# Kernel tuning notes

Measured on AMD Instinct MI355X. Metric: run time of the kernel, lower is better.

## Reference

```python
import jax, jax.numpy as jnp
from jax import lax
import numpy as np

DN = ('NDHWC', 'DHWIO', 'NDHWC')

def _conv(x, W):
    # stride-1 kernel-3 sparse conv on dense grid: SAME conv; absent voxels are zero
    return lax.conv_general_dilated(x, W, (1, 1, 1), 'SAME', dimension_numbers=DN)

def _tconv(x, W):
    # kernel-2 stride-2 generative transpose conv: exactly doubles each spatial dim
    return lax.conv_transpose(x, W, (2, 2, 2), 'VALID', dimension_numbers=DN)

def _pool(h):
    B, D1, D2, D3, C = h.shape
    return h.reshape(B, D1 // 2, 2, D2 // 2, 2, D3 // 2, 2, C).max(axis=(2, 4, 6))

def _pool_mask(m):
    B, D1, D2, D3 = m.shape
    return m.reshape(B, D1 // 2, 2, D2 // 2, 2, D3 // 2, 2).max(axis=(2, 4, 6))

def _up_mask(m):
    return jnp.repeat(jnp.repeat(jnp.repeat(m, 2, axis=1), 2, axis=2), 2, axis=3)

def setup_inputs() -> dict:
    key = jax.random.key(0)
    ks = jax.random.split(key, 6)
    B, G = 2, 128
    x = jax.random.normal(ks[0], (B, G, G, G, 1), dtype=jnp.float32)
    occ = jax.random.randint(ks[1], (B, G, G, G), 0, 10, dtype=jnp.int32)
    def xavier(k, shape):
        fan_in = np.prod(shape[:-1]); fan_out = shape[-1]
        std = np.sqrt(2.0 / (fan_in + fan_out)).astype(np.float32)
        return jax.random.normal(k, shape, dtype=jnp.float32) * std
    W1 = xavier(ks[2], (3, 3, 3, 1, 16))
    W2 = xavier(ks[3], (3, 3, 3, 16, 4))
    Wt1 = xavier(ks[4], (2, 2, 2, 4, 16))
    Wt2 = xavier(ks[5], (2, 2, 2, 16, 1))
    return {"x": x, "W1": W1, "W2": W2, "Wt1": Wt1, "Wt2": Wt2, "occ": occ}

def reference(x, W1, W2, Wt1, Wt2, occ):
    m0 = (occ == 0).astype(x.dtype)            # occupancy mask at full res
    xm = x * m0[..., None]
    h = jax.nn.relu(_conv(xm, W1)) * m0[..., None]   # coords unchanged
    h = _pool(h); m1 = _pool_mask(m0)                # stride-2 max pool on sparse coords
    h = jax.nn.relu(_conv(h, W2)) * m1[..., None]
    h = _pool(h); m2 = _pool_mask(m1)
    m3 = _up_mask(m2)                                # transpose conv emits all children coords
    h = jax.nn.relu(_tconv(h, Wt1)) * m3[..., None]
    m4 = _up_mask(m3)
    out = jax.nn.sigmoid(_tconv(h, Wt2)) * m4[..., None]
    return out
```

## Files before the change

### kernel.cpp

```cpp
#include <hip/hip_runtime.h>
#include <hip/hip_fp16.h>

#define G 128

typedef _Float16 h2_t __attribute__((ext_vector_type(2)));

union U16 { uint4 u; h2_t h2[4]; };
union HV  { uint4 u; h2_t h2[4]; };

__device__ __forceinline__ float dot2f(h2_t a, h2_t b, float c) {
#if __has_builtin(__builtin_amdgcn_fdot2)
    return __builtin_amdgcn_fdot2(a, b, c, false);
#else
    return c + (float)a.x * (float)b.x + (float)a.y * (float)b.y;
#endif
}

__device__ __forceinline__ h2_t h2max(h2_t a, h2_t b) {
#if __has_builtin(__builtin_elementwise_max)
    return __builtin_elementwise_max(a, b);
#else
    h2_t r;
    r.x = a.x > b.x ? a.x : b.x;
    r.y = a.y > b.y ? a.y : b.y;
    return r;
#endif
}

__global__ void k_prep(const float* __restrict__ W1, const float* __restrict__ W2,
                       __half* __restrict__ w1h, __half* __restrict__ w2h)
{
    int i = blockIdx.x * 256 + threadIdx.x;
    if (i < 216) {
        int tap = i >> 3, p = i & 7;
        w1h[2 * i]     = __float2half(W1[tap * 16 + 2 * p]);
        w1h[2 * i + 1] = __float2half(W1[tap * 16 + 2 * p + 1]);
    }
    if (i < 864) {
        int t = i >> 5, r = i & 31, co = r >> 3, p = r & 7;
        w2h[2 * i]     = __float2half(W2[t * 64 + (2 * p) * 4 + co]);
        w2h[2 * i + 1] = __float2half(W2[t * 64 + (2 * p + 1) * 4 + co]);
    }
}

__global__ __launch_bounds__(256, 4)
void k_conv1_pool(const float* __restrict__ x, const int* __restrict__ occ,
                  const h2_t* __restrict__ w1h,
                  __half* __restrict__ h1p, float* __restrict__ m1)
{
    __shared__ _Float16      sx[10 * 18 * 18];
    __shared__ unsigned char sm[10 * 18 * 18];

    const int bx = blockIdx.x, by = blockIdx.y;
    const int b  = blockIdx.z >> 4, zt = blockIdx.z & 15;
    const int tid = threadIdx.x;

    const int z0 = zt * 8 - 1, y0 = by * 16 - 1, x0 = bx * 16 - 1;
    const int base_b = b * G * G * G;

    #pragma unroll
    for (int r = 0; r < 13; ++r) {
        int i = r * 256 + tid;
        if (i < 3240) {
            int lz = i / 324, rr = i - lz * 324;
            int ly = rr / 18, lx = rr - ly * 18;
            int gz = z0 + lz, gy = y0 + ly, gx = x0 + lx;
            bool inb = (unsigned)gz < 128u && (unsigned)gy < 128u &&
                       (unsigned)gx < 128u;
            int oc = 1; float xv = 0.f;
            if (inb) {
                int gi = base_b + (gz * G + gy) * G + gx;
                oc = occ[gi];
                xv = x[gi];
            }
            bool mm = inb && (oc == 0);
            sx[i] = mm ? (_Float16)xv : (_Float16)0.f;
            sm[i] = mm ? 1 : 0;
        }
    }
    __syncthreads();

    const int tx = tid & 7, ty = (tid >> 3) & 7, tz = tid >> 6;

    const h2_t zero = (h2_t)(_Float16)0.f;
    h2_t best[8];
    #pragma unroll
    for (int c = 0; c < 8; ++c) best[c] = zero;
    int anym = 0;

    #pragma unroll
    for (int pos = 0; pos < 8; ++pos) {
        const int dz = pos >> 2, dy = (pos >> 1) & 1, dx = pos & 1;
        const int cz = 2 * tz + dz, cy = 2 * ty + dy, cx = 2 * tx + dx;
        const int cb = (cz + 1) * 324 + (cy + 1) * 18 + (cx + 1);
        if (sm[cb]) {
            anym = 1;
            h2_t acc[8];
            #pragma unroll
            for (int c = 0; c < 8; ++c) acc[c] = zero;
            #pragma unroll
            for (int kz = 0; kz < 3; ++kz)
            #pragma unroll
            for (int ky = 0; ky < 3; ++ky)
            #pragma unroll
            for (int kx = 0; kx < 3; ++kx) {
                _Float16 v = sx[cb + (kz - 1) * 324 + (ky - 1) * 18 + (kx - 1)];
                h2_t v2 = {v, v};
                const h2_t* w = &w1h[((kz * 3 + ky) * 3 + kx) * 8];
                #pragma unroll
                for (int c = 0; c < 8; ++c) acc[c] = v2 * w[c] + acc[c];
            }
            #pragma unroll
            for (int c = 0; c < 8; ++c) best[c] = h2max(best[c], h2max(acc[c], zero));
        }
    }

    const int pz = zt * 4 + tz, py = by * 8 + ty, px = bx * 8 + tx;
    const int vidx = ((b * 64 + pz) * 64 + py) * 64 + px;
    HV p0, p1;
    #pragma unroll
    for (int c = 0; c < 4; ++c) { p0.h2[c] = best[c]; p1.h2[c] = best[4 + c]; }
    uint4* o = (uint4*)&h1p[(size_t)vidx * 16];
    o[0] = p0.u;
    o[1] = p1.u;
    m1[vidx] = anym ? 1.f : 0.f;
}

__global__ __launch_bounds__(128)
void k_conv2_pool(const __half* __restrict__ h1p, const float* __restrict__ m1,
                  const h2_t* __restrict__ w2h,
                  float* __restrict__ h2, float* __restrict__ m2)
{
    __shared__ uint4 tile[660];

    const int bx = blockIdx.x, by = blockIdx.y;
    const int b  = blockIdx.z >> 4, z4 = blockIdx.z & 15;
    const int tid = threadIdx.x;

    const int z0 = z4 * 4 - 1, y0 = by * 8 - 1, x0 = bx * 8 - 1;

    const int dy = tid & 1, dz = (tid >> 1) & 1;
    const int qx = (tid >> 2) & 3, Y = (tid >> 4) & 3, Z = (tid >> 6) & 1;
    const int cx0 = 2 * qx, cy = 2 * Y + dy, cz = 2 * Z + dz;

    float acc[2][4] = {{0.f, 0.f, 0.f, 0.f}, {0.f, 0.f, 0.f, 0.f}};

    for (int h = 0; h < 2; ++h) {
        if (h) __syncthreads();
        #pragma unroll
        for (int it = 0; it < 6; ++it) {
            int g = it * 128 + tid;
            if (g < 660) {
                int z = g / 110, r = g - z * 110, y = r / 11, xx = r - y * 11;
                int gz = z0 + z, gy = y0 + y, gx = x0 + xx;
                uint4 a = make_uint4(0u, 0u, 0u, 0u);
                if ((unsigned)gz < 64u && (unsigned)gy < 64u && (unsigned)gx < 64u)
                    a = ((const uint4*)&h1p[(size_t)(((b * 64 + gz) * 64 + gy) * 64 + gx) * 16])[h];
                tile[g] = a;
            }
        }
        __syncthreads();

        #pragma unroll
        for (int kz = 0; kz < 3; ++kz)
        #pragma unroll
        for (int ky = 0; ky < 3; ++ky) {
            const int rb = (cz + kz) * 110 + (cy + ky) * 11 + cx0;
            h2_t hp[4][4];
            #pragma unroll
            for (int xi = 0; xi < 4; ++xi) {
                U16 a; a.u = tile[rb + xi];
                #pragma unroll
                for (int p = 0; p < 4; ++p) hp[xi][p] = a.h2[p];
            }
            const int t3 = (kz * 3 + ky) * 3;
            #pragma unroll
            for (int kx = 0; kx < 3; ++kx) {
                const h2_t* w = w2h + (t3 + kx) * 32 + 4 * h;
                #pragma unroll
                for (int j = 0; j < 2; ++j) {
                    #pragma unroll
                    for (int co = 0; co < 4; ++co) {
                        float a = acc[j][co];
                        #pragma unroll
                        for (int p = 0; p < 4; ++p)
                            a = dot2f(hp[kx + j][p], w[co * 8 + p], a);
                        acc[j][co] = a;
                    }
                }
            }
        }
    }

    const int gcz = z4 * 4 + cz, gcy = by * 8 + cy, gcx = bx * 8 + cx0;
    const float mv0 = m1[((b * 64 + gcz) * 64 + gcy) * 64 + gcx];
    const float mv1 = m1[((b * 64 + gcz) * 64 + gcy) * 64 + gcx + 1];
    float m = fmaxf(mv0, mv1);
    float r0 = fmaxf(fmaxf(acc[0][0], 0.f) * mv0, fmaxf(acc[1][0], 0.f) * mv1);
    float r1 = fmaxf(fmaxf(acc[0][1], 0.f) * mv0, fmaxf(acc[1][1], 0.f) * mv1);
    float r2 = fmaxf(fmaxf(acc[0][2], 0.f) * mv0, fmaxf(acc[1][2], 0.f) * mv1);
    float r3 = fmaxf(fmaxf(acc[0][3], 0.f) * mv0, fmaxf(acc[1][3], 0.f) * mv1);

    #pragma unroll
    for (int mask = 1; mask <= 2; mask <<= 1) {
        r0 = fmaxf(r0, __shfl_xor(r0, mask));
        r1 = fmaxf(r1, __shfl_xor(r1, mask));
        r2 = fmaxf(r2, __shfl_xor(r2, mask));
        r3 = fmaxf(r3, __shfl_xor(r3, mask));
        m  = fmaxf(m,  __shfl_xor(m,  mask));
    }
    if ((tid & 3) == 0) {
        int pz = z4 * 2 + Z, py = by * 4 + Y, px = bx * 4 + qx;
        int oidx = ((b * 32 + pz) * 32 + py) * 32 + px;
        *(float4*)&h2[oidx * 4] = make_float4(r0, r1, r2, r3);
        m2[oidx] = m;
    }
}

__device__ __forceinline__ float dot4(float4 a, float4 b) {
    return a.x * b.x + a.y * b.y + a.z * b.z + a.w * b.w;
}

__global__ __launch_bounds__(256)
void k_decoder(const float* __restrict__ h2, const float* __restrict__ m2,
               const float* __restrict__ Wt1, const float* __restrict__ Wt2,
               float* __restrict__ out)
{
    __shared__ float4 w1s[256];
    __shared__ float4 w2s[32];

    const int tid = threadIdx.x;
    w1s[tid] = ((const float4*)Wt1)[tid];
    if (tid < 32) w2s[tid] = ((const float4*)Wt2)[tid];
    __syncthreads();

    const int T  = blockIdx.x * 256 + tid;
    const int px = T & 31;
    const int a  = (T >> 5) & 1;
    const int bb = (T >> 6) & 1;
    const int py = (T >> 7) & 31;
    const int pz = (T >> 12) & 31;
    const int b  = T >> 17;
    const int pidx = ((b * 32 + pz) * 32 + py) * 32 + px;

    const float m = m2[pidx];
    const float4 hv = *(const float4*)&h2[pidx * 4];

    const int b0q = ((((1 - a) * 2 + (1 - bb)) * 2) + 1) * 16;
    const int b1q = ((((1 - a) * 2 + (1 - bb)) * 2) + 0) * 16;
    float4 t0q[4], t1q[4];
    #pragma unroll
    for (int q = 0; q < 4; ++q) {
        float4 a0 = w1s[b0q + q],      a1 = w1s[b0q + 4 + q];
        float4 a2 = w1s[b0q + 8 + q],  a3 = w1s[b0q + 12 + q];
        float4 c0 = w1s[b1q + q],      c1 = w1s[b1q + 4 + q];
        float4 c2 = w1s[b1q + 8 + q],  c3 = w1s[b1q + 12 + q];
        float4 s0, s1;
        s0.x = hv.x * a0.x + hv.y * a1.x + hv.z * a2.x + hv.w * a3.x;
        s0.y = hv.x * a0.y + hv.y * a1.y + hv.z * a2.y + hv.w * a3.y;
        s0.z = hv.x * a0.z + hv.y * a1.z + hv.z * a2.z + hv.w * a3.z;
        s0.w = hv.x * a0.w + hv.y * a1.w + hv.z * a2.w + hv.w * a3.w;
        s1.x = hv.x * c0.x + hv.y * c1.x + hv.z * c2.x + hv.w * c3.x;
        s1.y = hv.x * c0.y + hv.y * c1.y + hv.z * c2.y + hv.w * c3.y;
        s1.z = hv.x * c0.z + hv.y * c1.z + hv.z * c2.z + hv.w * c3.z;
        s1.w = hv.x * c0.w + hv.y * c1.w + hv.z * c2.w + hv.w * c3.w;
        t0q[q] = make_float4(fmaxf(s0.x, 0.f), fmaxf(s0.y, 0.f),
                             fmaxf(s0.z, 0.f), fmaxf(s0.w, 0.f));
        t1q[q] = make_float4(fmaxf(s1.x, 0.f), fmaxf(s1.y, 0.f),
                             fmaxf(s1.z, 0.f), fmaxf(s1.w, 0.f));
    }

    #pragma unroll
    for (int e = 0; e < 2; ++e) {
        #pragma unroll
        for (int f = 0; f < 2; ++f) {
            const int d  = 4 * pz + 2 * a + e;
            const int hh = 4 * py + 2 * bb + f;
            const int be = ((1 - e) * 2 + (1 - f)) * 2;
            const float4* wg0 = &w2s[(be + 1) * 4];
            const float4* wg1 = &w2s[(be + 0) * 4];
            float s00 = dot4(t0q[0], wg0[0]) + dot4(t0q[1], wg0[1])
                      + dot4(t0q[2], wg0[2]) + dot4(t0q[3], wg0[3]);
            float s01 = dot4(t0q[0], wg1[0]) + dot4(t0q[1], wg1[1])
                      + dot4(t0q[2], wg1[2]) + dot4(t0q[3], wg1[3]);
            float s10 = dot4(t1q[0], wg0[0]) + dot4(t1q[1], wg0[1])
                      + dot4(t1q[2], wg0[2]) + dot4(t1q[3], wg0[3]);
            float s11 = dot4(t1q[0], wg1[0]) + dot4(t1q[1], wg1[1])
                      + dot4(t1q[2], wg1[2]) + dot4(t1q[3], wg1[3]);
            float4 o;
            o.x = m / (1.f + __expf(-s00));
            o.y = m / (1.f + __expf(-s01));
            o.z = m / (1.f + __expf(-s10));
            o.w = m / (1.f + __expf(-s11));
            *(float4*)&out[((b * G + d) * G + hh) * G + 4 * px] = o;
        }
    }
}

extern "C" void kernel_launch(void* const* d_in, const int* in_sizes, int n_in,
                              void* d_out, int out_size, void* d_ws, size_t ws_size,
                              hipStream_t stream) {
    (void)in_sizes; (void)n_in; (void)out_size; (void)ws_size;
    const float* x   = (const float*)d_in[0];
    const float* W1  = (const float*)d_in[1];
    const float* W2  = (const float*)d_in[2];
    const float* Wt1 = (const float*)d_in[3];
    const float* Wt2 = (const float*)d_in[4];
    const int*   occ = (const int*)d_in[5];
    float* out = (float*)d_out;

    char* ws = (char*)d_ws;
    __half* h1p = (__half*)ws;
    float*  m1  = (float*)(ws + 8388608ull * sizeof(__half));
    float*  h2  = m1 + 524288;
    float*  m2v = h2 + 262144;
    __half* w2h = (__half*)(m2v + 65536);
    __half* w1h = w2h + 1728;

    k_prep<<<dim3(4), dim3(256), 0, stream>>>(W1, W2, w1h, w2h);
    k_conv1_pool<<<dim3(8, 8, 32), dim3(256), 0, stream>>>(x, occ, (const h2_t*)w1h, h1p, m1);
    k_conv2_pool<<<dim3(8, 8, 32), dim3(128), 0, stream>>>(h1p, m1, (const h2_t*)w2h, h2, m2v);
    k_decoder<<<dim3(1024), dim3(256), 0, stream>>>(h2, m2v, Wt1, Wt2, out);
}
```

Measured before the change: 168.5 us.

## Fuse conv2+pool with transpose-conv decoder into one kernel

Merges the second conv/pool kernel and the decoder kernel into one kernel. Each 256-thread block now covers a deeper z tile, keeps the pooled features and mask in shared memory, and immediately runs both transpose convolutions and the sigmoid for its region. This removes one launch and the global round trip of the intermediate h2/m2 buffers, and reduces halo overhead in z. The trade-off is a less coalesced output store pattern, since each row is now written in small 64-byte chunks. The conv1 launch-bounds occupancy hint is also lowered from 4 to 2.

```diff
diff --git a/kernel.cpp b/kernel.cpp
--- a/kernel.cpp
+++ b/kernel.cpp
@@ -27,6 +27,10 @@
 #endif
 }
 
+__device__ __forceinline__ float dot4(float4 a, float4 b) {
+    return a.x * b.x + a.y * b.y + a.z * b.z + a.w * b.w;
+}
+
 __global__ void k_prep(const float* __restrict__ W1, const float* __restrict__ W2,
                        __half* __restrict__ w1h, __half* __restrict__ w2h)
 {
@@ -43,7 +47,7 @@
     }
 }
 
-__global__ __launch_bounds__(256, 4)
+__global__ __launch_bounds__(256, 2)
 void k_conv1_pool(const float* __restrict__ x, const int* __restrict__ occ,
                   const h2_t* __restrict__ w1h,
                   __half* __restrict__ h1p, float* __restrict__ m1)
@@ -126,21 +130,29 @@
     m1[vidx] = anym ? 1.f : 0.f;
 }
 
-__global__ __launch_bounds__(128)
-void k_conv2_pool(const __half* __restrict__ h1p, const float* __restrict__ m1,
-                  const h2_t* __restrict__ w2h,
-                  float* __restrict__ h2, float* __restrict__ m2)
+__global__ __launch_bounds__(256)
+void k_conv2_dec(const __half* __restrict__ h1p, const float* __restrict__ m1,
+                 const h2_t* __restrict__ w2h,
+                 const float* __restrict__ Wt1, const float* __restrict__ Wt2,
+                 float* __restrict__ out)
 {
-    __shared__ uint4 tile[660];
+    __shared__ uint4  tile[1100];
+    __shared__ float4 wt1[128];
+    __shared__ float4 wt2[32];
+    __shared__ float4 sh_h[64];
+    __shared__ float  sh_m[64];
 
     const int bx = blockIdx.x, by = blockIdx.y;
-    const int b  = blockIdx.z >> 4, z4 = blockIdx.z & 15;
+    const int b  = blockIdx.z >> 3, bz = blockIdx.z & 7;
     const int tid = threadIdx.x;
 
-    const int z0 = z4 * 4 - 1, y0 = by * 8 - 1, x0 = bx * 8 - 1;
+    if (tid < 128) wt1[tid] = ((const float4*)Wt1)[tid];
+    if (tid < 32)  wt2[tid] = ((const float4*)Wt2)[tid];
+
+    const int z0 = bz * 8 - 1, y0 = by * 8 - 1, x0 = bx * 8 - 1;
 
     const int dy = tid & 1, dz = (tid >> 1) & 1;
-    const int qx = (tid >> 2) & 3, Y = (tid >> 4) & 3, Z = (tid >> 6) & 1;
+    const int qx = (tid >> 2) & 3, Y = (tid >> 4) & 3, Z = (tid >> 6) & 3;
     const int cx0 = 2 * qx, cy = 2 * Y + dy, cz = 2 * Z + dz;
 
     float acc[2][4] = {{0.f, 0.f, 0.f, 0.f}, {0.f, 0.f, 0.f, 0.f}};
@@ -148,9 +160,9 @@
     for (int h = 0; h < 2; ++h) {
         if (h) __syncthreads();
         #pragma unroll
-        for (int it = 0; it < 6; ++it) {
-            int g = it * 128 + tid;
-            if (g < 660) {
+        for (int it = 0; it < 5; ++it) {
+            int g = it * 256 + tid;
+            if (g < 1100) {
                 int z = g / 110, r = g - z * 110, y = r / 11, xx = r - y * 11;
                 int gz = z0 + z, gy = y0 + y, gx = x0 + xx;
                 uint4 a = make_uint4(0u, 0u, 0u, 0u);
@@ -192,7 +204,7 @@
         }
     }
 
-    const int gcz = z4 * 4 + cz, gcy = by * 8 + cy, gcx = bx * 8 + cx0;
+    const int gcz = bz * 8 + cz, gcy = by * 8 + cy, gcx = bx * 8 + cx0;
     const float mv0 = m1[((b * 64 + gcz) * 64 + gcy) * 64 + gcx];
     const float mv1 = m1[((b * 64 + gcz) * 64 + gcy) * 64 + gcx + 1];
     float m = fmaxf(mv0, mv1);
@@ -210,89 +222,70 @@
         m  = fmaxf(m,  __shfl_xor(m,  mask));
     }
     if ((tid & 3) == 0) {
-        int pz = z4 * 2 + Z, py = by * 4 + Y, px = bx * 4 + qx;
-        int oidx = ((b * 32 + pz) * 32 + py) * 32 + px;
-        *(float4*)&h2[oidx * 4] = make_float4(r0, r1, r2, r3);
-        m2[oidx] = m;
-    }
-}
-
-__device__ __forceinline__ float dot4(float4 a, float4 b) {
-    return a.x * b.x + a.y * b.y + a.z * b.z + a.w * b.w;
-}
-
-__global__ __launch_bounds__(256)
-void k_decoder(const float* __restrict__ h2, const float* __restrict__ m2,
-               const float* __restrict__ Wt1, const float* __restrict__ Wt2,
-               float* __restrict__ out)
-{
-    __shared__ float4 w1s[256];
-    __shared__ float4 w2s[32];
-
-    const int tid = threadIdx.x;
-    w1s[tid] = ((const float4*)Wt1)[tid];
-    if (tid < 32) w2s[tid] = ((const float4*)Wt2)[tid];
+        int p = Z * 16 + Y * 4 + qx;
+        sh_h[p] = make_float4(r0, r1, r2, r3);
+        sh_m[p] = m;
+    }
     __syncthreads();
 
-    const int T  = blockIdx.x * 256 + tid;
-    const int px = T & 31;
-    const int a  = (T >> 5) & 1;
-    const int bb = (T >> 6) & 1;
-    const int py = (T >> 7) & 31;
-    const int pz = (T >> 12) & 31;
-    const int b  = T >> 17;
-    const int pidx = ((b * 32 + pz) * 32 + py) * 32 + px;
-
-    const float m = m2[pidx];
-    const float4 hv = *(const float4*)&h2[pidx * 4];
-
-    const int b0q = ((((1 - a) * 2 + (1 - bb)) * 2) + 1) * 16;
-    const int b1q = ((((1 - a) * 2 + (1 - bb)) * 2) + 0) * 16;
-    float4 t0q[4], t1q[4];
-    #pragma unroll
-    for (int q = 0; q < 4; ++q) {
-        float4 a0 = w1s[b0q + q],      a1 = w1s[b0q + 4 + q];
-        float4 a2 = w1s[b0q + 8 + q],  a3 = w1s[b0q + 12 + q];
-        float4 c0 = w1s[b1q + q],      c1 = w1s[b1q + 4 + q];
-        float4 c2 = w1s[b1q + 8 + q],  c3 = w1s[b1q + 12 + q];
-        float4 s0, s1;
-        s0.x = hv.x * a0.x + hv.y * a1.x + hv.z * a2.x + hv.w * a3.x;
-        s0.y = hv.x * a0.y + hv.y * a1.y + hv.z * a2.y + hv.w * a3.y;
-        s0.z = hv.x * a0.z + hv.y * a1.z + hv.z * a2.z + hv.w * a3.z;
-        s0.w = hv.x * a0.w + hv.y * a1.w + hv.z * a2.w + hv.w * a3.w;
-        s1.x = hv.x * c0.x + hv.y * c1.x + hv.z * c2.x + hv.w * c3.x;
-        s1.y = hv.x * c0.y + hv.y * c1.y + hv.z * c2.y + hv.w * c3.y;
-        s1.z = hv.x * c0.z + hv.y * c1.z + hv.z * c2.z + hv.w * c3.z;
-        s1.w = hv.x * c0.w + hv.y * c1.w + hv.z * c2.w + hv.w * c3.w;
-        t0q[q] = make_float4(fmaxf(s0.x, 0.f), fmaxf(s0.y, 0.f),
-                             fmaxf(s0.z, 0.f), fmaxf(s0.w, 0.f));
-        t1q[q] = make_float4(fmaxf(s1.x, 0.f), fmaxf(s1.y, 0.f),
-                             fmaxf(s1.z, 0.f), fmaxf(s1.w, 0.f));
-    }
-
-    #pragma unroll
-    for (int e = 0; e < 2; ++e) {
-        #pragma unroll
-        for (int f = 0; f < 2; ++f) {
-            const int d  = 4 * pz + 2 * a + e;
-            const int hh = 4 * py + 2 * bb + f;
-            const int be = ((1 - e) * 2 + (1 - f)) * 2;
-            const float4* wg0 = &w2s[(be + 1) * 4];
-            const float4* wg1 = &w2s[(be + 0) * 4];
-            float s00 = dot4(t0q[0], wg0[0]) + dot4(t0q[1], wg0[1])
-                      + dot4(t0q[2], wg0[2]) + dot4(t0q[3], wg0[3]);
-            float s01 = dot4(t0q[0], wg1[0]) + dot4(t0q[1], wg1[1])
-                      + dot4(t0q[2], wg1[2]) + dot4(t0q[3], wg1[3]);
-            float s10 = dot4(t1q[0], wg0[0]) + dot4(t1q[1], wg0[1])
-                      + dot4(t1q[2], wg0[2]) + dot4(t1q[3], wg0[3]);
-            float s11 = dot4(t1q[0], wg1[0]) + dot4(t1q[1], wg1[1])
-                      + dot4(t1q[2], wg1[2]) + dot4(t1q[3], wg1[3]);
-            float4 o;
-            o.x = m / (1.f + __expf(-s00));
-            o.y = m / (1.f + __expf(-s01));
-            o.z = m / (1.f + __expf(-s10));
-            o.w = m / (1.f + __expf(-s11));
-            *(float4*)&out[((b * G + d) * G + hh) * G + 4 * px] = o;
+    {
+        const int p  = tid >> 2;
+        const int a  = (tid >> 1) & 1;
+        const int bb = tid & 1;
+        const int pZ = p >> 4, pY = (p >> 2) & 3, pq = p & 3;
+        const int pz = bz * 4 + pZ, py = by * 4 + pY, pxq = bx * 4 + pq;
+
+        const float mm = sh_m[p];
+        const float4 hv = sh_h[p];
+
+        const int b0q = ((((1 - a) * 2 + (1 - bb)) * 2) + 1) * 16;
+        const int b1q = ((((1 - a) * 2 + (1 - bb)) * 2) + 0) * 16;
+        float4 t0q[4], t1q[4];
+        #pragma unroll
+        for (int q = 0; q < 4; ++q) {
+            float4 a0 = wt1[b0q + q],      a1 = wt1[b0q + 4 + q];
+            float4 a2 = wt1[b0q + 8 + q],  a3 = wt1[b0q + 12 + q];
+            float4 c0 = wt1[b1q + q],      c1 = wt1[b1q + 4 + q];
+            float4 c2 = wt1[b1q + 8 + q],  c3 = wt1[b1q + 12 + q];
+            float4 s0, s1;
+            s0.x = hv.x * a0.x + hv.y * a1.x + hv.z * a2.x + hv.w * a3.x;
+            s0.y = hv.x * a0.y + hv.y * a1.y + hv.z * a2.y + hv.w * a3.y;
+            s0.z = hv.x * a0.z + hv.y * a1.z + hv.z * a2.z + hv.w * a3.z;
+            s0.w = hv.x * a0.w + hv.y * a1.w + hv.z * a2.w + hv.w * a3.w;
+            s1.x = hv.x * c0.x + hv.y * c1.x + hv.z * c2.x + hv.w * c3.x;
+            s1.y = hv.x * c0.y + hv.y * c1.y + hv.z * c2.y + hv.w * c3.y;
+            s1.z = hv.x * c0.z + hv.y * c1.z + hv.z * c2.z + hv.w * c3.z;
+            s1.w = hv.x * c0.w + hv.y * c1.w + hv.z * c2.w + hv.w * c3.w;
+            t0q[q] = make_float4(fmaxf(s0.x, 0.f), fmaxf(s0.y, 0.f),
+                                 fmaxf(s0.z, 0.f), fmaxf(s0.w, 0.f));
+            t1q[q] = make_float4(fmaxf(s1.x, 0.f), fmaxf(s1.y, 0.f),
+                                 fmaxf(s1.z, 0.f), fmaxf(s1.w, 0.f));
+        }
+
+        #pragma unroll
+        for (int e = 0; e < 2; ++e) {
+            #pragma unroll
+            for (int f = 0; f < 2; ++f) {
+                const int d  = 4 * pz + 2 * a + e;
+                const int hh = 4 * py + 2 * bb + f;
+                const int be = ((1 - e) * 2 + (1 - f)) * 2;
+                const float4* wg0 = &wt2[(be + 1) * 4];
+                const float4* wg1 = &wt2[(be + 0) * 4];
+                float s00 = dot4(t0q[0], wg0[0]) + dot4(t0q[1], wg0[1])
+                          + dot4(t0q[2], wg0[2]) + dot4(t0q[3], wg0[3]);
+                float s01 = dot4(t0q[0], wg1[0]) + dot4(t0q[1], wg1[1])
+                          + dot4(t0q[2], wg1[2]) + dot4(t0q[3], wg1[3]);
+                float s10 = dot4(t1q[0], wg0[0]) + dot4(t1q[1], wg0[1])
+                          + dot4(t1q[2], wg0[2]) + dot4(t1q[3], wg0[3]);
+                float s11 = dot4(t1q[0], wg1[0]) + dot4(t1q[1], wg1[1])
+                          + dot4(t1q[2], wg1[2]) + dot4(t1q[3], wg1[3]);
+                float4 o;
+                o.x = mm / (1.f + __expf(-s00));
+                o.y = mm / (1.f + __expf(-s01));
+                o.z = mm / (1.f + __expf(-s10));
+                o.w = mm / (1.f + __expf(-s11));
+                *(float4*)&out[((b * G + d) * G + hh) * G + 4 * pxq] = o;
+            }
         }
     }
 }
@@ -312,13 +305,10 @@
     char* ws = (char*)d_ws;
     __half* h1p = (__half*)ws;
     float*  m1  = (float*)(ws + 8388608ull * sizeof(__half));
-    float*  h2  = m1 + 524288;
-    float*  m2v = h2 + 262144;
-    __half* w2h = (__half*)(m2v + 65536);
+    __half* w2h = (__half*)(m1 + 524288);
     __half* w1h = w2h + 1728;
 
     k_prep<<<dim3(4), dim3(256), 0, stream>>>(W1, W2, w1h, w2h);
     k_conv1_pool<<<dim3(8, 8, 32), dim3(256), 0, stream>>>(x, occ, (const h2_t*)w1h, h1p, m1);
-    k_conv2_pool<<<dim3(8, 8, 32), dim3(128), 0, stream>>>(h1p, m1, (const h2_t*)w2h, h2, m2v);
-    k_decoder<<<dim3(1024), dim3(256), 0, stream>>>(h2, m2v, Wt1, Wt2, out);
-}
+    k_conv2_dec<<<dim3(8, 8, 16), dim3(256), 0, stream>>>(h1p, m1, (const h2_t*)w2h, Wt1, Wt2, out);
+}
```

Result: no change. 166.3 us (-1.3%).
